# Kernel tuning notes

Hardware: AMD Instinct MI355X
Metric: run time of the kernel (lower is better)

## Reference

```python
import jax, jax.numpy as jnp
import numpy as np

TEMPERATURE = 0.07
BASE_TEMPERATURE = 0.07


def setup_inputs() -> dict:
    key = jax.random.key(0)
    k1, k2 = jax.random.split(key)
    N, D = 8192, 512
    features = jax.random.normal(k1, (N, D), dtype=jnp.float32)
    labels = jax.random.randint(k2, (N,), 0, 64, dtype=jnp.int64 if jax.config.jax_enable_x64 else jnp.int32)
    return {"features": features, "labels": labels, "rotation_multiplier": 2}


def reference(features, labels, rotation_multiplier):
    k = int(rotation_multiplier)
    N = features.shape[0]
    B = N // k
    # L2-normalize rows (torch F.normalize clamps norm at eps=1e-12)
    norm = jnp.maximum(jnp.linalg.norm(features, axis=1, keepdims=True), 1e-12)
    f = features / norm
    sim = jnp.matmul(f, f.T) / TEMPERATURE  # [N, N]

    # block positive mask: groups of k rows share a label; compare group labels
    lab = labels.reshape(B, k)[:, 0]  # [B]
    same = lab[:, None] == lab[None, :]  # [B, B]
    mask = jnp.repeat(jnp.repeat(same, k, axis=0), k, axis=1)  # [N, N]
    eye = jnp.eye(N, dtype=bool)
    mask = mask & ~eye

    # stable masked log-softmax with diagonal removed from denominator
    logits_max = jax.lax.stop_gradient(jnp.max(sim, axis=1, keepdims=True))
    logits = sim - logits_max
    exp_logits = jnp.exp(logits)
    denom = exp_logits.sum(axis=1, keepdims=True) - jnp.diagonal(exp_logits)[:, None] + 1e-8
    log_prob = logits - jnp.log(denom)

    mask_f = mask.astype(logits.dtype)
    mask_sum = mask_f.sum(axis=1)  # [N]
    valid = mask_sum > 0
    mean_log_prob_pos = (log_prob * mask_f).sum(axis=1) / jnp.maximum(mask_sum, 1.0)
    per_sample = -(TEMPERATURE / BASE_TEMPERATURE) * mean_log_prob_pos
    n_valid = valid.sum().astype(logits.dtype)
    loss = jnp.where(valid, per_sample, 0.0).sum() / jnp.maximum(n_valid, 1.0)
    return loss
```

## Files before the change

### kernel.cpp

```cpp
#include <hip/hip_runtime.h>
#include <hip/hip_bf16.h>

#define TEMP_INV 14.285714285714286f
#define FSCALE 16.0f
#define T1S (TEMP_INV / 256.0f)

typedef __attribute__((ext_vector_type(4))) float f32x4;
typedef __attribute__((ext_vector_type(2))) long lx2;

#define ASYNC_COPY16(gp, lp)                                                  \
  __builtin_amdgcn_global_load_lds(                                          \
      (__attribute__((address_space(1))) const void*)(gp),                    \
      (__attribute__((address_space(3))) void*)(lp), 16, 0, 0)

__global__ __launch_bounds__(256) void norm_label_k(const float* __restrict__ feat,
                                                    uchar* __restrict__ fq,
                                                    const int* __restrict__ labels,
                                                    const int* __restrict__ kptr,
                                                    int* __restrict__ glab,
                                                    int* __restrict__ cnt,
                                                    float* __restrict__ gacc,
                                                    int* __restrict__ dcnt,
                                                    int N, int D) {
  const int row = (blockIdx.x * 256 + threadIdx.x) >> 6;
  const int lane = threadIdx.x & 63;
  if (row < N) {
    const float4* fr = (const float4*)(feat + (size_t)row * D);
    float4 v0 = fr[lane * 2];
    float4 v1 = fr[lane * 2 + 1];
    float ss = v0.x * v0.x + v0.y * v0.y + v0.z * v0.z + v0.w * v0.w +
               v1.x * v1.x + v1.y * v1.y + v1.z * v1.z + v1.w * v1.w;
    #pragma unroll
    for (int off = 32; off; off >>= 1) ss += __shfl_xor(ss, off, 64);
    const float inv = FSCALE / fmaxf(sqrtf(ss), 1e-12f);
    int w0 = 0, w1 = 0;
    w0 = __builtin_amdgcn_cvt_pk_fp8_f32(v0.x * inv, v0.y * inv, w0, false);
    w0 = __builtin_amdgcn_cvt_pk_fp8_f32(v0.z * inv, v0.w * inv, w0, true);
    w1 = __builtin_amdgcn_cvt_pk_fp8_f32(v1.x * inv, v1.y * inv, w1, false);
    w1 = __builtin_amdgcn_cvt_pk_fp8_f32(v1.z * inv, v1.w * inv, w1, true);
    uint2 o; o.x = (uint)w0; o.y = (uint)w1;
    const int pofs = (lane >> 4) * 128 + (lane & 3) * 32 + ((lane >> 2) & 3) * 8;
    *(uint2*)(fq + (size_t)row * D + pofs) = o;
  }
  if (blockIdx.x == 0) {
    const int k = *kptr;
    const int B = N / k;
    __shared__ int h[64];
    const int t = threadIdx.x;
    if (t < 2) gacc[t] = 0.f;
    if (t == 2) *dcnt = 0;
    if (t < 64) h[t] = 0;
    __syncthreads();
    for (int b = t; b < B; b += 256) {
      int lb = labels[(size_t)b * k];
      if (lb >= 0 && lb < 64) atomicAdd(&h[lb], 1);
    }
    __syncthreads();
    if (t < 64) cnt[t] = h[t];
    for (int i = t; i < N; i += 256) glab[i] = labels[(size_t)(i / k) * k];
  }
}

__global__ __launch_bounds__(256, 4) void gemm_k(const uchar* __restrict__ fq,
                                                 const int* __restrict__ glab,
                                                 float* __restrict__ part,
                                                 int N, int D) {
  __shared__ uchar As[128 * 128];
  __shared__ uchar Bs[128 * 128];
  const int t = threadIdx.x;
  const int lane = t & 63;
  const int wid = t >> 6;
  const int wrow = wid >> 1, wcol = wid & 1;
  const int quad = lane >> 4, l15 = lane & 15;

  const int nb = N / 128;
  const int total = nb * (nb + 1) / 2;
  int gidx = blockIdx.x;
  if ((total & 7) == 0) {
    const int per = total >> 3;
    gidx = (blockIdx.x & 7) * per + (blockIdx.x >> 3);
  }
  int idx = gidx, bi = 0;
  while (idx >= nb - bi) { idx -= nb - bi; bi++; }
  const int bj = bi + idx;
  const int i0 = bi * 128, j0 = bj * 128;
  const bool diagblk = (bi == bj);

  f32x4 acc[4][4];
  #pragma unroll
  for (int mi = 0; mi < 4; mi++)
    #pragma unroll
    for (int ni = 0; ni < 4; ni++) {
      f32x4 z = {0.f, 0.f, 0.f, 0.f};
      acc[mi][ni] = z;
    }

  uchar* sb = (wid < 2) ? As : Bs;
  const int rbase = (wid & 1) * 64;
  const int rowstart = ((wid < 2) ? i0 : j0) + rbase;
  const int lrow = lane >> 3;
  const int lch = lane & 7;

  for (int kb = 0; kb < D; kb += 128) {
    __syncthreads();
    #pragma unroll
    for (int i = 0; i < 8; i++) {
      const int rl = 8 * i + lrow;
      const int cg = lch ^ (rl & 7);
      ASYNC_COPY16(fq + (size_t)(rowstart + rl) * D + kb + cg * 16,
                   sb + (rbase + 8 * i) * 128);
    }
    __syncthreads();
    #pragma unroll
    for (int t2 = 0; t2 < 2; t2++) {
      lx2 a2[4], b2[4];
      #pragma unroll
      for (int mi = 0; mi < 4; mi++) {
        const int r = wrow * 64 + mi * 16 + l15;
        a2[mi] = *(const lx2*)&As[r * 128 + (((2 * quad + t2) ^ (r & 7)) << 4)];
      }
      #pragma unroll
      for (int ni = 0; ni < 4; ni++) {
        const int r = wcol * 64 + ni * 16 + l15;
        b2[ni] = *(const lx2*)&Bs[r * 128 + (((2 * quad + t2) ^ (r & 7)) << 4)];
      }
      #pragma unroll
      for (int mi = 0; mi < 4; mi++)
        #pragma unroll
        for (int ni = 0; ni < 4; ni++) {
          acc[mi][ni] = __builtin_amdgcn_mfma_f32_16x16x32_fp8_fp8(a2[mi][0], b2[ni][0], acc[mi][ni], 0, 0, 0);
          acc[mi][ni] = __builtin_amdgcn_mfma_f32_16x16x32_fp8_fp8(a2[mi][1], b2[ni][1], acc[mi][ni], 0, 0, 0);
        }
    }
  }

  __syncthreads();
  float* sf = (float*)As;
  const int colbase = j0 + wcol * 64 + l15;
  int clab[4];
  #pragma unroll
  for (int ni = 0; ni < 4; ni++) clab[ni] = glab[colbase + ni * 16];

  float colE[4] = {0.f, 0.f, 0.f, 0.f};
  float colP[4] = {0.f, 0.f, 0.f, 0.f};

  #pragma unroll
  for (int mi = 0; mi < 4; mi++) {
    const int lrw = wrow * 64 + mi * 16 + quad * 4;
    #pragma unroll
    for (int r = 0; r < 4; r++) {
      const int row = i0 + lrw + r;
      const int rlab = glab[row];
      float Ssum = 0.f, Psum = 0.f;
      #pragma unroll
      for (int ni = 0; ni < 4; ni++) {
        const int col = colbase + ni * 16;
        const float val = acc[mi][ni][r];
        const float lg = fmaf(val, T1S, -TEMP_INV);
        const bool diag = diagblk && (row == col);
        const float e = diag ? 0.f : __expf(lg);
        const float pm = (!diag && rlab == clab[ni]) ? lg : 0.f;
        Ssum += e; Psum += pm;
        colE[ni] += e; colP[ni] += pm;
      }
      #pragma unroll
      for (int off = 8; off; off >>= 1) {
        Ssum += __shfl_xor(Ssum, off, 64);
        Psum += __shfl_xor(Psum, off, 64);
      }
      if (l15 == 0) {
        sf[wcol * 128 + lrw + r]       = Ssum;
        sf[256 + wcol * 128 + lrw + r] = Psum;
      }
    }
  }
  if (!diagblk) {
    #pragma unroll
    for (int ni = 0; ni < 4; ni++) {
      float e = colE[ni];
      float p = colP[ni];
      e += __shfl_xor(e, 16, 64);
      e += __shfl_xor(e, 32, 64);
      p += __shfl_xor(p, 16, 64);
      p += __shfl_xor(p, 32, 64);
      const int lcol = wcol * 64 + ni * 16 + l15;
      if (quad == 0) {
        sf[512 + wrow * 128 + lcol] = e;
        sf[768 + wrow * 128 + lcol] = p;
      }
    }
  }
  __syncthreads();
  float* dst = part + (size_t)gidx * 512;
  if (t < 128) {
    dst[t]       = sf[t] + sf[128 + t];
    dst[128 + t] = sf[256 + t] + sf[384 + t];
  } else if (!diagblk) {
    const int u = t - 128;
    dst[256 + u] = sf[512 + u] + sf[640 + u];
    dst[384 + u] = sf[768 + u] + sf[896 + u];
  }
}

__global__ __launch_bounds__(128) void reduce_loss_k(const float* __restrict__ part,
                                                     const int* __restrict__ glab,
                                                     const int* __restrict__ cnt,
                                                     const int* __restrict__ kptr,
                                                     float* __restrict__ gacc,
                                                     int* __restrict__ dcnt,
                                                     float* __restrict__ out, int N) {
  const int nb = N / 128;
  const int b = blockIdx.x;
  const int t = threadIdx.x;
  const int i = b * 128 + t;
  float S = 0.f, P = 0.f;
  const int base = b * nb - b * (b - 1) / 2;
  for (int bj = b; bj < nb; bj++) {
    const float* p = part + (size_t)(base + bj - b) * 512;
    S += p[t];
    P += p[128 + t];
  }
  for (int bi = 0; bi < b; bi++) {
    const int idx = bi * nb - bi * (bi - 1) / 2 + (b - bi);
    const float* p = part + (size_t)idx * 512;
    S += p[256 + t];
    P += p[384 + t];
  }
  const int k = *kptr;
  const int np = cnt[glab[i]] * k - 1;
  float l = 0.f, v = 0.f;
  if (np > 0) {
    l = -(P - (float)np * logf(S + 1e-8f)) / (float)np;
    v = 1.f;
  }
  #pragma unroll
  for (int off = 32; off; off >>= 1) {
    l += __shfl_xor(l, off, 64);
    v += __shfl_xor(v, off, 64);
  }
  __shared__ float sl[2], sv[2];
  if ((t & 63) == 0) { sl[t >> 6] = l; sv[t >> 6] = v; }
  __syncthreads();
  if (t == 0) {
    atomicAdd(&gacc[0], sl[0] + sl[1]);
    atomicAdd(&gacc[1], sv[0] + sv[1]);
    __threadfence();
    const int prev = atomicAdd(dcnt, 1);
    if (prev == (int)gridDim.x - 1) {
      const float L = atomicAdd(&gacc[0], 0.f);
      const float V = atomicAdd(&gacc[1], 0.f);
      out[0] = L / fmaxf(V, 1.f);
    }
  }
}

extern "C" void kernel_launch(void* const* d_in, const int* in_sizes, int n_in,
                              void* d_out, int out_size, void* d_ws, size_t ws_size,
                              hipStream_t stream) {
  const float* feat = (const float*)d_in[0];
  const int* labels = (const int*)d_in[1];
  const int* kptr   = (const int*)d_in[2];
  const int N = in_sizes[1];
  const int D = in_sizes[0] / N;

  const int nb = N / 128;
  const int total = nb * (nb + 1) / 2;

  char* ws = (char*)d_ws;
  uchar* fq = (uchar*)ws;
  size_t off = (size_t)N * D;
  float* part = (float*)(ws + off); off += (size_t)total * 512 * sizeof(float);
  int* glab   = (int*)(ws + off);   off += (size_t)N * sizeof(int);
  int* cnt    = (int*)(ws + off);   off += 64 * sizeof(int);
  float* gacc = (float*)(ws + off); off += 2 * sizeof(float);
  int* dcnt   = (int*)(ws + off);   off += sizeof(int);

  norm_label_k<<<(N + 3) / 4, 256, 0, stream>>>(feat, fq, labels, kptr, glab, cnt,
                                                gacc, dcnt, N, D);
  gemm_k<<<total, 256, 0, stream>>>(fq, glab, part, N, D);
  reduce_loss_k<<<nb, 128, 0, stream>>>(part, glab, cnt, kptr, gacc, dcnt,
                                        (float*)d_out, N);
}
```

Baseline: 149.8 us.

## Use gfx950 scaled 16x16x128 FP8 MFMA and parallelize loss reduction across slices

The GEMM inner loop now loads two 16-byte K chunks per row into a 32-byte operand and issues one MFMA-scale 16x16x128 f8f6f4 instruction in place of four 16x16x32 FP8 MFMAs. The unit scale exponent 127 keeps the numerics unchanged. The aim is fewer MFMA issues and higher matrix-core throughput on MI355X, at the cost of more operand registers per instruction. Separately, the final reduction kernel uses 512 threads that split the partial-tile loop four ways and combine the results through shared memory, to shorten the serial per-thread accumulation.

```diff
diff --git a/kernel.cpp b/kernel.cpp
--- a/kernel.cpp
+++ b/kernel.cpp
@@ -6,7 +6,8 @@
 #define T1S (TEMP_INV / 256.0f)
 
 typedef __attribute__((ext_vector_type(4))) float f32x4;
-typedef __attribute__((ext_vector_type(2))) long lx2;
+typedef __attribute__((ext_vector_type(4))) int i32x4;
+typedef __attribute__((ext_vector_type(8))) int i32x8;
 
 #define ASYNC_COPY16(gp, lp)                                                  \
   __builtin_amdgcn_global_load_lds(                                          \
@@ -111,26 +112,24 @@
                    sb + (rbase + 8 * i) * 128);
     }
     __syncthreads();
-    #pragma unroll
-    for (int t2 = 0; t2 < 2; t2++) {
-      lx2 a2[4], b2[4];
-      #pragma unroll
-      for (int mi = 0; mi < 4; mi++) {
-        const int r = wrow * 64 + mi * 16 + l15;
-        a2[mi] = *(const lx2*)&As[r * 128 + (((2 * quad + t2) ^ (r & 7)) << 4)];
-      }
-      #pragma unroll
-      for (int ni = 0; ni < 4; ni++) {
-        const int r = wcol * 64 + ni * 16 + l15;
-        b2[ni] = *(const lx2*)&Bs[r * 128 + (((2 * quad + t2) ^ (r & 7)) << 4)];
-      }
+    i32x8 av[4];
+    #pragma unroll
+    for (int mi = 0; mi < 4; mi++) {
+      const int r = wrow * 64 + mi * 16 + l15;
+      i32x4 lo = *(const i32x4*)&As[r * 128 + (((2 * quad) ^ (r & 7)) << 4)];
+      i32x4 hi = *(const i32x4*)&As[r * 128 + (((2 * quad + 1) ^ (r & 7)) << 4)];
+      av[mi] = (i32x8){lo.x, lo.y, lo.z, lo.w, hi.x, hi.y, hi.z, hi.w};
+    }
+    #pragma unroll
+    for (int ni = 0; ni < 4; ni++) {
+      const int r = wcol * 64 + ni * 16 + l15;
+      i32x4 lo = *(const i32x4*)&Bs[r * 128 + (((2 * quad) ^ (r & 7)) << 4)];
+      i32x4 hi = *(const i32x4*)&Bs[r * 128 + (((2 * quad + 1) ^ (r & 7)) << 4)];
+      i32x8 bv = (i32x8){lo.x, lo.y, lo.z, lo.w, hi.x, hi.y, hi.z, hi.w};
       #pragma unroll
       for (int mi = 0; mi < 4; mi++)
-        #pragma unroll
-        for (int ni = 0; ni < 4; ni++) {
-          acc[mi][ni] = __builtin_amdgcn_mfma_f32_16x16x32_fp8_fp8(a2[mi][0], b2[ni][0], acc[mi][ni], 0, 0, 0);
-          acc[mi][ni] = __builtin_amdgcn_mfma_f32_16x16x32_fp8_fp8(a2[mi][1], b2[ni][1], acc[mi][ni], 0, 0, 0);
-        }
+        acc[mi][ni] = __builtin_amdgcn_mfma_scale_f32_16x16x128_f8f6f4(
+            av[mi], bv, acc[mi][ni], 0, 0, 0, 127, 0, 127);
     }
   }
 
@@ -202,7 +201,7 @@
   }
 }
 
-__global__ __launch_bounds__(128) void reduce_loss_k(const float* __restrict__ part,
+__global__ __launch_bounds__(512) void reduce_loss_k(const float* __restrict__ part,
                                                      const int* __restrict__ glab,
                                                      const int* __restrict__ cnt,
                                                      const int* __restrict__ kptr,
@@ -211,45 +210,56 @@
                                                      float* __restrict__ out, int N) {
   const int nb = N / 128;
   const int b = blockIdx.x;
-  const int t = threadIdx.x;
-  const int i = b * 128 + t;
+  const int t = threadIdx.x & 127;
+  const int sl = threadIdx.x >> 7;
   float S = 0.f, P = 0.f;
   const int base = b * nb - b * (b - 1) / 2;
-  for (int bj = b; bj < nb; bj++) {
+  for (int bj = b + sl; bj < nb; bj += 4) {
     const float* p = part + (size_t)(base + bj - b) * 512;
     S += p[t];
     P += p[128 + t];
   }
-  for (int bi = 0; bi < b; bi++) {
+  for (int bi = sl; bi < b; bi += 4) {
     const int idx = bi * nb - bi * (bi - 1) / 2 + (b - bi);
     const float* p = part + (size_t)idx * 512;
     S += p[256 + t];
     P += p[384 + t];
   }
-  const int k = *kptr;
-  const int np = cnt[glab[i]] * k - 1;
+  __shared__ float sS[4][128], sP[4][128];
+  sS[sl][t] = S; sP[sl][t] = P;
+  __syncthreads();
   float l = 0.f, v = 0.f;
-  if (np > 0) {
-    l = -(P - (float)np * logf(S + 1e-8f)) / (float)np;
-    v = 1.f;
+  if (sl == 0) {
+    S = sS[0][t] + sS[1][t] + sS[2][t] + sS[3][t];
+    P = sP[0][t] + sP[1][t] + sP[2][t] + sP[3][t];
+    const int k = *kptr;
+    const int np = cnt[glab[b * 128 + t]] * k - 1;
+    if (np > 0) {
+      l = -(P - (float)np * logf(S + 1e-8f)) / (float)np;
+      v = 1.f;
+    }
   }
   #pragma unroll
   for (int off = 32; off; off >>= 1) {
     l += __shfl_xor(l, off, 64);
     v += __shfl_xor(v, off, 64);
   }
-  __shared__ float sl[2], sv[2];
-  if ((t & 63) == 0) { sl[t >> 6] = l; sv[t >> 6] = v; }
-  __syncthreads();
-  if (t == 0) {
-    atomicAdd(&gacc[0], sl[0] + sl[1]);
-    atomicAdd(&gacc[1], sv[0] + sv[1]);
+  __shared__ float sl8[8], sv8[8];
+  const int tt = threadIdx.x;
+  if ((tt & 63) == 0) { sl8[tt >> 6] = l; sv8[tt >> 6] = v; }
+  __syncthreads();
+  if (tt == 0) {
+    float L = 0.f, V = 0.f;
+    #pragma unroll
+    for (int i = 0; i < 8; i++) { L += sl8[i]; V += sv8[i]; }
+    atomicAdd(&gacc[0], L);
+    atomicAdd(&gacc[1], V);
     __threadfence();
     const int prev = atomicAdd(dcnt, 1);
     if (prev == (int)gridDim.x - 1) {
-      const float L = atomicAdd(&gacc[0], 0.f);
-      const float V = atomicAdd(&gacc[1], 0.f);
-      out[0] = L / fmaxf(V, 1.f);
+      const float Lf = atomicAdd(&gacc[0], 0.f);
+      const float Vf = atomicAdd(&gacc[1], 0.f);
+      out[0] = Lf / fmaxf(Vf, 1.f);
     }
   }
 }
@@ -278,6 +288,6 @@
   norm_label_k<<<(N + 3) / 4, 256, 0, stream>>>(feat, fq, labels, kptr, glab, cnt,
                                                 gacc, dcnt, N, D);
   gemm_k<<<total, 256, 0, stream>>>(fq, glab, part, N, D);
-  reduce_loss_k<<<nb, 128, 0, stream>>>(part, glab, cnt, kptr, gacc, dcnt,
+  reduce_loss_k<<<nb, 512, 0, stream>>>(part, glab, cnt, kptr, gacc, dcnt,
                                         (float*)d_out, N);
 }
```

After: 135.8 us. 1.1x faster.
